# Performance work log

Measured on AMD Instinct MI355X. Metric: run time of the kernel, lower is better.

## Reference

```python
import jax, jax.numpy as jnp
import numpy as np

EPS = 0.05
ITERS = 100
TOL = 1e-4
LN_EPS = 1e-5


def _ln(x, s, b):
    m = x.mean(-1, keepdims=True)
    v = ((x - m) ** 2).mean(-1, keepdims=True)
    return (x - m) / jnp.sqrt(v + LN_EPS) * s + b


def _sinkhorn(M):
    # M: [N, HW] raw logits (fp32). Entropic OT with uniform marginals.
    n, hw = M.shape
    log_K = M / EPS
    log_mu = jnp.log(1.0 / n + 1e-8)
    log_nu = jnp.log(1.0 / hw + 1e-8)

    def cond(st):
        i, lu, lv, diff = st
        return (i < ITERS) & (diff >= TOL)

    def body(st):
        i, lu, lv, _ = st
        new_lu = log_mu - jax.scipy.special.logsumexp(log_K + lv[None, :], axis=1)
        new_lv = log_nu - jax.scipy.special.logsumexp(log_K + new_lu[:, None], axis=0)
        return (i + 1, new_lu, new_lv, jnp.max(jnp.abs(new_lu - lu)))

    st0 = (jnp.int32(0), jnp.zeros((n,), jnp.float32), jnp.zeros((hw,), jnp.float32), jnp.float32(jnp.inf))
    _, lu, lv, _ = jax.lax.while_loop(cond, body, st0)
    log_T = lu[:, None] + log_K + lv[None, :]
    return jnp.clip(jnp.exp(log_T), 0.0, 1.0)


def setup_inputs() -> dict:
    key = jax.random.key(0)
    ks = jax.random.split(key, 12)
    B, C, H, W, N = 16, 256, 64, 64, 5
    E = 2 * C
    w = lambda k, sh: (jax.random.normal(k, sh, jnp.float32) * 0.02)
    return {
        'Fd': jax.random.normal(ks[0], (B, C, H, W), jnp.float32),
        'prompts': w(ks[1], (N, C)),
        'sa_q_w': w(ks[2], (C, C)), 'sa_q_b': jnp.zeros((C,), jnp.float32),
        'sa_k_w': w(ks[3], (C, C)), 'sa_k_b': jnp.zeros((C,), jnp.float32),
        'sa_v_w': w(ks[4], (C, C)), 'sa_v_b': jnp.zeros((C,), jnp.float32),
        'sa_ln_s': jnp.ones((C,), jnp.float32), 'sa_ln_b': jnp.zeros((C,), jnp.float32),
        'wq_w': w(ks[5], (C, C)), 'wq_b': jnp.zeros((C,), jnp.float32),
        'wk_w': w(ks[6], (C, C)), 'wk_b': jnp.zeros((C,), jnp.float32),
        'wv_w': w(ks[7], (C, C)), 'wv_b': jnp.zeros((C,), jnp.float32),
        'ca_ln_s': jnp.ones((C,), jnp.float32), 'ca_ln_b': jnp.zeros((C,), jnp.float32),
        'ffn_w1': w(ks[8], (C, E)), 'ffn_b1': jnp.zeros((E,), jnp.float32),
        'ffn_w2': w(ks[9], (E, C)), 'ffn_b2': jnp.zeros((C,), jnp.float32),
        'ffn_ln_s': jnp.ones((C,), jnp.float32), 'ffn_ln_b': jnp.zeros((C,), jnp.float32),
    }


def reference(Fd, prompts, sa_q_w, sa_q_b, sa_k_w, sa_k_b, sa_v_w, sa_v_b,
              sa_ln_s, sa_ln_b, wq_w, wq_b, wk_w, wk_b, wv_w, wv_b,
              ca_ln_s, ca_ln_b, ffn_w1, ffn_b1, ffn_w2, ffn_b2, ffn_ln_s, ffn_ln_b):
    B, C, H, W = Fd.shape
    scale = C ** -0.5
    Fd_flat = Fd.transpose(0, 2, 3, 1).reshape(B, H * W, C)  # [B, HW, C]
    P = jnp.broadcast_to(prompts[None], (B,) + prompts.shape)  # [B, N, C]

    # self-attention over prompts
    Q = P @ sa_q_w + sa_q_b
    K = P @ sa_k_w + sa_k_b
    V = P @ sa_v_w + sa_v_b
    attn = jax.nn.softmax(jnp.einsum('bnc,bmc->bnm', Q, K) * scale, axis=-1)
    P = _ln(P + jnp.einsum('bnm,bmc->bnc', attn, V), sa_ln_s, sa_ln_b)

    # cross-attention prompts -> pixels
    Qc = P @ wq_w + wq_b                 # [B, N, C]
    Kc = Fd_flat @ wk_w + wk_b           # [B, HW, C]
    Vc = Fd_flat @ wv_w + wv_b           # [B, HW, C]
    logits = jnp.einsum('bnc,bmc->bnm', Qc, Kc) * scale  # [B, N, HW]
    M = jax.nn.softmax(logits, axis=-1)
    P = _ln(P + jnp.einsum('bnm,bmc->bnc', M, Vc), ca_ln_s, ca_ln_b)

    # OT regularization: Sinkhorn on detached logits, BCE(M, T*)
    T = jax.vmap(_sinkhorn)(jax.lax.stop_gradient(logits))
    Mc = jnp.clip(M, 1e-6, 1.0 - 1e-6)
    bce = -(T * jnp.log(Mc) + (1.0 - T) * jnp.log(1.0 - Mc))
    L_ot = bce.mean(axis=(1, 2)).mean()

    # FFN + residual + LN
    h = jax.nn.gelu(P @ ffn_w1 + ffn_b1, approximate=False) @ ffn_w2 + ffn_b2
    P_hat = _ln(P + h, ffn_ln_s, ffn_ln_b)
    return (P_hat, L_ot)
```

## Files before the change

kernel.cpp:

```cpp
#include <hip/hip_runtime.h>
#include <hip/hip_fp16.h>
#include <math.h>

#define LOG2E 1.44269504088896340f
#define LN2   0.69314718055994531f

__device__ __forceinline__ float warpReduceSum(float v){
#pragma unroll
    for (int off = 32; off > 0; off >>= 1) v += __shfl_down(v, off);
    return v;
}
__device__ __forceinline__ float warpReduceMax(float v){
#pragma unroll
    for (int off = 32; off > 0; off >>= 1) v = fmaxf(v, __shfl_down(v, off));
    return v;
}

__device__ float blockSum256(float v, float* s4){
    v = warpReduceSum(v);
    int w = threadIdx.x >> 6;
    __syncthreads();
    if ((threadIdx.x & 63) == 0) s4[w] = v;
    __syncthreads();
    return s4[0] + s4[1] + s4[2] + s4[3];
}
__device__ float blockSum512(float v, float* s8){
    v = warpReduceSum(v);
    int w = threadIdx.x >> 6;
    __syncthreads();
    if ((threadIdx.x & 63) == 0) s8[w] = v;
    __syncthreads();
    float s = 0.f;
#pragma unroll
    for (int i = 0; i < 8; i++) s += s8[i];
    return s;
}

__global__ __launch_bounds__(256) void k_qkv(
    const float* __restrict__ prompts,
    const float* __restrict__ qw, const float* __restrict__ qb,
    const float* __restrict__ kw, const float* __restrict__ kb,
    const float* __restrict__ vw, const float* __restrict__ vb,
    float* __restrict__ QKV)
{
    __shared__ float Pl[1280];
    __shared__ float parts[4][5][64];
    int t = threadIdx.x;
    int mat = blockIdx.x >> 2, chunk = blockIdx.x & 3;
    for (int i = t; i < 1280; i += 256) Pl[i] = prompts[i];
    const float* W  = (mat == 0) ? qw : (mat == 1) ? kw : vw;
    const float* Bv = (mat == 0) ? qb : (mat == 1) ? kb : vb;
    int cl = t & 63, p = t >> 6;
    int col = chunk*64 + cl;
    __syncthreads();
    float acc[5] = {0,0,0,0,0};
    const float* wp = W + (size_t)(p*64)*256 + col;
#pragma unroll 8
    for (int c = 0; c < 64; c++){
        float wv = wp[(size_t)c*256];
#pragma unroll
        for (int n = 0; n < 5; n++) acc[n] += Pl[n*256 + p*64 + c] * wv;
    }
#pragma unroll
    for (int n = 0; n < 5; n++) parts[p][n][cl] = acc[n];
    __syncthreads();
    for (int i = t; i < 320; i += 256){
        int n = i >> 6, c2 = i & 63;
        float s = parts[0][n][c2] + parts[1][n][c2] + parts[2][n][c2] + parts[3][n][c2]
                + Bv[chunk*64 + c2];
        QKV[mat*1280 + n*256 + chunk*64 + c2] = s;
    }
}

__global__ __launch_bounds__(256) void k_attn_qc(
    const float* __restrict__ QKV, const float* __restrict__ prompts,
    const float* __restrict__ lns, const float* __restrict__ lnb,
    const float* __restrict__ wqw, const float* __restrict__ wqb,
    float* __restrict__ P1g, float* __restrict__ Qcg)
{
    __shared__ float Pl[1280], Ql[1280], Kl[1280], Vl[1280], Sl[25], s4[4];
    int t = threadIdx.x;
    for (int i = t; i < 1280; i += 256){
        Pl[i] = prompts[i];
        Ql[i] = QKV[i];
        Kl[i] = QKV[1280 + i];
        Vl[i] = QKV[2560 + i];
    }
    __syncthreads();
    if (t < 25){
        int n = t / 5, m = t % 5;
        float s = 0.f;
        for (int c = 0; c < 256; c++) s += Ql[n*256 + c] * Kl[m*256 + c];
        Sl[t] = s * 0.0625f;
    }
    __syncthreads();
    if (t < 5){
        float mx = -1e30f;
        for (int m = 0; m < 5; m++) mx = fmaxf(mx, Sl[t*5 + m]);
        float e[5], sm = 0.f;
        for (int m = 0; m < 5; m++){ e[m] = expf(Sl[t*5 + m] - mx); sm += e[m]; }
        for (int m = 0; m < 5; m++) Sl[t*5 + m] = e[m] / sm;
    }
    __syncthreads();
    float x[5];
#pragma unroll
    for (int n = 0; n < 5; n++){
        float s = 0.f;
        for (int m = 0; m < 5; m++) s += Sl[n*5 + m] * Vl[m*256 + t];
        x[n] = Pl[n*256 + t] + s;
    }
#pragma unroll
    for (int n = 0; n < 5; n++){
        float sum  = blockSum256(x[n], s4);
        float mean = sum * (1.0f/256.0f);
        float d    = x[n] - mean;
        float sq   = blockSum256(d*d, s4);
        float rstd = rsqrtf(sq * (1.0f/256.0f) + 1e-5f);
        float y = d * rstd * lns[t] + lnb[t];
        Pl[n*256 + t] = y;
        if (blockIdx.x == 0) P1g[n*256 + t] = y;
    }
    __syncthreads();
    int n = blockIdx.x;
    float acc = wqb[t];
    const float* wp = wqw + t;
#pragma unroll 16
    for (int d = 0; d < 256; d++) acc += Pl[n*256 + d] * wp[(size_t)d*256];
    Qcg[n*256 + t] = acc;
}

__global__ __launch_bounds__(256) void k_qk2(
    const float* __restrict__ Qc, const float* __restrict__ wkw,
    const float* __restrict__ wkb,
    float* __restrict__ qkg, float* __restrict__ qkbg)
{
    __shared__ float Qr[256], s4[4];
    int n = blockIdx.y, t = threadIdx.x;
    int w = t >> 6, lane = t & 63;
    Qr[t] = Qc[n*256 + t];
    __syncthreads();
#pragma unroll
    for (int i = 0; i < 4; i++){
        int c = blockIdx.x*16 + w*4 + i;
        const float* kp = wkw + (size_t)c*256;
        float acc = Qr[lane]       * kp[lane]
                  + Qr[lane + 64]  * kp[lane + 64]
                  + Qr[lane + 128] * kp[lane + 128]
                  + Qr[lane + 192] * kp[lane + 192];
#pragma unroll
        for (int off = 1; off < 64; off <<= 1) acc += __shfl_xor(acc, off);
        if (lane == 0) qkg[n*256 + c] = acc;
    }
    if (blockIdx.x == 0){
        float pu = blockSum256(Qr[t] * wkb[t], s4);
        if (t == 0) qkbg[n] = pu;
    }
}

__global__ __launch_bounds__(1024) void k_logits(
    const float* __restrict__ Fd, const float* __restrict__ qkg,
    const float* __restrict__ qkbg, float* __restrict__ logits)
{
    __shared__ float qk[1280];
    __shared__ float qb5[5];
    __shared__ float parts[4][5][256];
    int t = threadIdx.x;
    for (int i = t; i < 1280; i += 1024) qk[i] = qkg[i];
    if (t < 5) qb5[t] = qkbg[t];
    __syncthreads();
    int b = blockIdx.y;
    int p = t >> 8, ml = t & 255;
    int m = blockIdx.x * 256 + ml;
    const float* fp = Fd + ((size_t)(b*256 + p*64)) * 4096 + m;
    float a0 = 0.f, a1 = 0.f, a2 = 0.f, a3 = 0.f, a4 = 0.f;
#pragma unroll 16
    for (int c = 0; c < 64; c++){
        float f = fp[(size_t)c * 4096];
        a0 += qk[          p*64 + c] * f;
        a1 += qk[256  +    p*64 + c] * f;
        a2 += qk[512  +    p*64 + c] * f;
        a3 += qk[768  +    p*64 + c] * f;
        a4 += qk[1024 +    p*64 + c] * f;
    }
    parts[p][0][ml] = a0; parts[p][1][ml] = a1; parts[p][2][ml] = a2;
    parts[p][3][ml] = a3; parts[p][4][ml] = a4;
    __syncthreads();
    for (int i = t; i < 1280; i += 1024){
        int n = i >> 8, mm = i & 255;
        float s = parts[0][n][mm] + parts[1][n][mm] + parts[2][n][mm] + parts[3][n][mm]
                + qb5[n];
        logits[((size_t)(b*5) + n)*4096 + blockIdx.x*256 + mm] = s * 0.0625f;
    }
}

__global__ __launch_bounds__(1024) void k_A(
    const float* __restrict__ Fd, const float* __restrict__ logits,
    float* __restrict__ A)
{
    __shared__ __align__(16) __half Ml[5*4096];
    __shared__ float red[80];
    int b = blockIdx.y, cc = blockIdx.x, t = threadIdx.x;
    int w = t >> 6, lane = t & 63;
    const float* Lb = logits + (size_t)(b*5) * 4096;
    float ll[5][4];
#pragma unroll
    for (int n = 0; n < 5; n++)
#pragma unroll
        for (int k = 0; k < 4; k++)
            ll[n][k] = Lb[n*4096 + t + k*1024];
#pragma unroll
    for (int n = 0; n < 5; n++){
        float tm = fmaxf(fmaxf(ll[n][0], ll[n][1]), fmaxf(ll[n][2], ll[n][3]));
        tm = warpReduceMax(tm);
        if (lane == 0) red[w*5 + n] = tm;
    }
    __syncthreads();
    float mx[5];
#pragma unroll
    for (int n = 0; n < 5; n++){
        float gm = -1e30f;
        for (int i = 0; i < 16; i++) gm = fmaxf(gm, red[i*5 + n]);
        mx[n] = gm;
    }
    __syncthreads();
    float e[5][4];
#pragma unroll
    for (int n = 0; n < 5; n++){
        float ps = 0.f;
#pragma unroll
        for (int k = 0; k < 4; k++){ e[n][k] = expf(ll[n][k] - mx[n]); ps += e[n][k]; }
        ps = warpReduceSum(ps);
        if (lane == 0) red[w*5 + n] = ps;
    }
    __syncthreads();
#pragma unroll
    for (int n = 0; n < 5; n++){
        float z = 0.f;
        for (int i = 0; i < 16; i++) z += red[i*5 + n];
        float inv = 1.0f / z;
#pragma unroll
        for (int k = 0; k < 4; k++)
            Ml[n*4096 + t + k*1024] = __float2half(e[n][k] * inv);
    }
    __syncthreads();
    int c = cc*16 + w;
    const float* fp = Fd + ((size_t)(b*256 + c)) * 4096;
    float4 a4[5];
#pragma unroll
    for (int n = 0; n < 5; n++) a4[n] = make_float4(0.f, 0.f, 0.f, 0.f);
#pragma unroll 4
    for (int it = 0; it < 16; it++){
        int m4 = it*256 + (lane << 2);
        float4 f = *(const float4*)(fp + m4);
#pragma unroll
        for (int n = 0; n < 5; n++){
            const __half2* mp = (const __half2*)(Ml + n*4096 + m4);
            float2 m0 = __half22float2(mp[0]);
            float2 m1 = __half22float2(mp[1]);
            a4[n].x += m0.x * f.x; a4[n].y += m0.y * f.y;
            a4[n].z += m1.x * f.z; a4[n].w += m1.y * f.w;
        }
    }
#pragma unroll
    for (int n = 0; n < 5; n++){
        float s = a4[n].x + a4[n].y + a4[n].z + a4[n].w;
        s = warpReduceSum(s);
        if (lane == 0) A[(size_t)(b*5 + n)*256 + c] = s;
    }
}

__global__ __launch_bounds__(1024) void k_sinkhorn(
    const float* __restrict__ logits, float* __restrict__ partial)
{
    __shared__ __align__(16) float redm[2][5][16];
    __shared__ __align__(16) float reds[5][16];
    __shared__ float redb[16];
    int b = blockIdx.x, t = threadIdx.x;
    int w = t >> 6, lane = t & 63;
    const float* Lb = logits + (size_t)b * 5 * 4096;
    float lk2[5][4], ek[5][4];
#pragma unroll
    for (int n = 0; n < 5; n++)
#pragma unroll
        for (int k = 0; k < 4; k++){
            float lv = (Lb[n*4096 + t + k*1024] / 0.05f) * LOG2E;
            lk2[n][k] = lv;
            ek[n][k] = exp2f(lv);
        }
    const float mu_lin  = 0.2f + 1e-8f;
    const float nu_lin  = 1.0f/4096.0f + 1e-8f;
    const float thr     = 1.00005e-4f;

    float vv[4]  = {1.f, 1.f, 1.f, 1.f};
    float en_prev[5] = {1.f, 1.f, 1.f, 1.f, 1.f};
    float en[5];
    float diff = 1e30f;
    int par = 0;

    for (int it = 0; it < 100; ++it){
        if (diff < 0.f) break;
        float gs[5];
#pragma unroll
        for (int n = 0; n < 5; n++)
            gs[n] = ek[n][0]*vv[0] + ek[n][1]*vv[1] + ek[n][2]*vv[2] + ek[n][3]*vv[3];
#pragma unroll
        for (int off = 1; off < 64; off <<= 1){
#pragma unroll
            for (int n = 0; n < 5; n++) gs[n] += __shfl_xor(gs[n], off);
        }
        if (lane == 0){
#pragma unroll
            for (int n = 0; n < 5; n++) redm[par][n][w] = gs[n];
        }
        __syncthreads();
        float slack = -1.f;
#pragma unroll
        for (int n = 0; n < 5; n++){
            const float4* rp = (const float4*)redm[par][n];
            float4 A4 = rp[0], B4 = rp[1], C4 = rp[2], D4 = rp[3];
            float s = (((A4.x+A4.y)+(A4.z+A4.w)) + ((B4.x+B4.y)+(B4.z+B4.w)))
                    + (((C4.x+C4.y)+(C4.z+C4.w)) + ((D4.x+D4.y)+(D4.z+D4.w)));
            float e = mu_lin / s;
            slack = fmaxf(slack, fabsf(e - en_prev[n]) - thr * en_prev[n]);
            en_prev[n] = e;
            en[n] = e;
        }
        diff = slack;
#pragma unroll
        for (int k = 0; k < 4; k++){
            float cs = ek[0][k]*en[0] + ek[1][k]*en[1] + ek[2][k]*en[2]
                     + ek[3][k]*en[3] + ek[4][k]*en[4];
            vv[k] = nu_lin / cs;
        }
        par ^= 1;
    }
    __syncthreads();

    float tm[5];
#pragma unroll
    for (int n = 0; n < 5; n++){
        float l0 = lk2[n][0]*0.05f, l1 = lk2[n][1]*0.05f;
        float l2 = lk2[n][2]*0.05f, l3 = lk2[n][3]*0.05f;
        tm[n] = fmaxf(fmaxf(l0, l1), fmaxf(l2, l3));
    }
#pragma unroll
    for (int off = 1; off < 64; off <<= 1){
#pragma unroll
        for (int n = 0; n < 5; n++) tm[n] = fmaxf(tm[n], __shfl_xor(tm[n], off));
    }
    if (lane == 0){
#pragma unroll
        for (int n = 0; n < 5; n++) redm[0][n][w] = tm[n];
    }
    __syncthreads();
    float mx5[5];
#pragma unroll
    for (int n = 0; n < 5; n++){
        const float4* rp = (const float4*)redm[0][n];
        float4 A4 = rp[0], B4 = rp[1], C4 = rp[2], D4 = rp[3];
        float gm = fmaxf(fmaxf(fmaxf(A4.x,A4.y), fmaxf(A4.z,A4.w)),
                         fmaxf(fmaxf(B4.x,B4.y), fmaxf(B4.z,B4.w)));
        gm = fmaxf(gm, fmaxf(fmaxf(fmaxf(C4.x,C4.y), fmaxf(C4.z,C4.w)),
                             fmaxf(fmaxf(D4.x,D4.y), fmaxf(D4.z,D4.w))));
        mx5[n] = gm;
    }
    float pz[5];
#pragma unroll
    for (int n = 0; n < 5; n++){
        pz[n] = exp2f(lk2[n][0]*0.05f - mx5[n]) + exp2f(lk2[n][1]*0.05f - mx5[n])
              + exp2f(lk2[n][2]*0.05f - mx5[n]) + exp2f(lk2[n][3]*0.05f - mx5[n]);
    }
#pragma unroll
    for (int off = 1; off < 64; off <<= 1){
#pragma unroll
        for (int n = 0; n < 5; n++) pz[n] += __shfl_xor(pz[n], off);
    }
    if (lane == 0){
#pragma unroll
        for (int n = 0; n < 5; n++) reds[n][w] = pz[n];
    }
    __syncthreads();
    float iz5[5];
#pragma unroll
    for (int n = 0; n < 5; n++){
        const float4* rp = (const float4*)reds[n];
        float4 A4 = rp[0], B4 = rp[1], C4 = rp[2], D4 = rp[3];
        float z = (((A4.x+A4.y)+(A4.z+A4.w)) + ((B4.x+B4.y)+(B4.z+B4.w)))
                + (((C4.x+C4.y)+(C4.z+C4.w)) + ((D4.x+D4.y)+(D4.z+D4.w)));
        iz5[n] = 1.0f / z;
    }
    float acc = 0.f;
#pragma unroll
    for (int n = 0; n < 5; n++){
#pragma unroll
        for (int k = 0; k < 4; k++){
            float Mv = exp2f(lk2[n][k]*0.05f - mx5[n]) * iz5[n];
            float Mc = fminf(fmaxf(Mv, 1e-6f), 1.0f - 1e-6f);
            float T  = fminf(en[n] * ek[n][k] * vv[k], 1.0f);
            acc -= (T * log2f(Mc) + (1.0f - T) * log2f(1.0f - Mc)) * LN2;
        }
    }
    acc = warpReduceSum(acc);
    if (lane == 0) redb[w] = acc;
    __syncthreads();
    if (t == 0){
        float s = 0.f;
        for (int i = 0; i < 16; i++) s += redb[i];
        partial[b] = s;
    }
}

__global__ __launch_bounds__(512) void k_epilogue(
    const float* __restrict__ A, const float* __restrict__ P1,
    const float* __restrict__ wvw, const float* __restrict__ wvb,
    const float* __restrict__ clns, const float* __restrict__ clnb,
    const float* __restrict__ w1, const float* __restrict__ b1,
    const float* __restrict__ w2, const float* __restrict__ b2,
    const float* __restrict__ flns, const float* __restrict__ flnb,
    const float* __restrict__ sink_part,
    float* __restrict__ out)
{
    __shared__ float Ar[256], P1r[256], P2[256], hl[512], parts[2][256], s8[8];
    int bn = blockIdx.x;
    int n = bn % 5;
    int t = threadIdx.x;
    if (bn == 0 && t == 0){
        float s = 0.f;
        for (int i = 0; i < 16; i++) s += sink_part[i];
        out[20480] = s * (1.0f / (16.0f * 5.0f * 4096.0f));
    }
    if (t < 256){ Ar[t] = A[(size_t)bn*256 + t]; P1r[t] = P1[n*256 + t]; }
    __syncthreads();
    int c = t & 255, p = t >> 8;
    {
        float acc = 0.f;
        const float* wp = wvw + (size_t)(p*128)*256 + c;
#pragma unroll 16
        for (int k = 0; k < 128; k++) acc += Ar[p*128 + k] * wp[(size_t)k*256];
        parts[p][c] = acc;
    }
    __syncthreads();
    float x = 0.f;
    if (t < 256) x = P1r[t] + parts[0][t] + parts[1][t] + wvb[t];
    float sum  = blockSum512((t < 256) ? x : 0.f, s8);
    float mean = sum * (1.0f/256.0f);
    float d    = x - mean;
    float sq   = blockSum512((t < 256) ? d*d : 0.f, s8);
    float rstd = rsqrtf(sq * (1.0f/256.0f) + 1e-5f);
    float p2v = 0.f;
    if (t < 256){
        p2v = d * rstd * clns[t] + clnb[t];
        P2[t] = p2v;
    }
    __syncthreads();
    {
        float a = b1[t];
        const float* wp = w1 + t;
#pragma unroll 16
        for (int k = 0; k < 256; k++) a += P2[k] * wp[(size_t)k*512];
        hl[t] = 0.5f * a * (1.0f + erff(a * 0.70710678118654752f));
    }
    __syncthreads();
    {
        float acc = 0.f;
        const float* wp = w2 + (size_t)(p*256)*256 + c;
#pragma unroll 16
        for (int k = 0; k < 256; k++) acc += hl[p*256 + k] * wp[(size_t)k*256];
        parts[p][c] = acc;
    }
    __syncthreads();
    float x2 = 0.f;
    if (t < 256) x2 = P2[t] + parts[0][t] + parts[1][t] + b2[t];
    float sum2  = blockSum512((t < 256) ? x2 : 0.f, s8);
    float mean2 = sum2 * (1.0f/256.0f);
    float d2    = x2 - mean2;
    float sq2   = blockSum512((t < 256) ? d2*d2 : 0.f, s8);
    float rstd2 = rsqrtf(sq2 * (1.0f/256.0f) + 1e-5f);
    if (t < 256) out[(size_t)bn*256 + t] = d2 * rstd2 * flns[t] + flnb[t];
}

extern "C" void kernel_launch(void* const* d_in, const int* in_sizes, int n_in,
                              void* d_out, int out_size, void* d_ws, size_t ws_size,
                              hipStream_t stream)
{
    const float* Fd      = (const float*)d_in[0];
    const float* prompts = (const float*)d_in[1];
    const float* sa_q_w  = (const float*)d_in[2];
    const float* sa_q_b  = (const float*)d_in[3];
    const float* sa_k_w  = (const float*)d_in[4];
    const float* sa_k_b  = (const float*)d_in[5];
    const float* sa_v_w  = (const float*)d_in[6];
    const float* sa_v_b  = (const float*)d_in[7];
    const float* sa_ln_s = (const float*)d_in[8];
    const float* sa_ln_b = (const float*)d_in[9];
    const float* wq_w    = (const float*)d_in[10];
    const float* wq_b    = (const float*)d_in[11];
    const float* wk_w    = (const float*)d_in[12];
    const float* wk_b    = (const float*)d_in[13];
    const float* wv_w    = (const float*)d_in[14];
    const float* wv_b    = (const float*)d_in[15];
    const float* ca_ln_s = (const float*)d_in[16];
    const float* ca_ln_b = (const float*)d_in[17];
    const float* ffn_w1  = (const float*)d_in[18];
    const float* ffn_b1  = (const float*)d_in[19];
    const float* ffn_w2  = (const float*)d_in[20];
    const float* ffn_b2  = (const float*)d_in[21];
    const float* ffn_ln_s= (const float*)d_in[22];
    const float* ffn_ln_b= (const float*)d_in[23];

    float* out = (float*)d_out;
    float* ws  = (float*)d_ws;

    float* P1     = ws;
    float* qkb    = ws + 1536;
    float* QKV    = ws + 2048;
    float* Qc     = ws + 6144;
    float* qkg    = ws + 8192;
    float* spart  = ws + 9472;
    float* logits = ws + 73728;
    float* Amat   = ws + 401408;

    k_qkv<<<12, 256, 0, stream>>>(prompts, sa_q_w, sa_q_b, sa_k_w, sa_k_b,
                                  sa_v_w, sa_v_b, QKV);
    k_attn_qc<<<5, 256, 0, stream>>>(QKV, prompts, sa_ln_s, sa_ln_b,
                                     wq_w, wq_b, P1, Qc);
    k_qk2<<<dim3(16, 5), 256, 0, stream>>>(Qc, wk_w, wk_b, qkg, qkb);
    k_logits<<<dim3(16, 16), 1024, 0, stream>>>(Fd, qkg, qkb, logits);
    k_A<<<dim3(16, 16), 1024, 0, stream>>>(Fd, logits, Amat);
    k_sinkhorn<<<16, 1024, 0, stream>>>(logits, spart);
    k_epilogue<<<80, 512, 0, stream>>>(Amat, P1, wv_w, wv_b, ca_ln_s, ca_ln_b,
                                       ffn_w1, ffn_b1, ffn_w2, ffn_b2,
                                       ffn_ln_s, ffn_ln_b, spart, out);
}
```

Measured before the change: 247.1 us.

## Merge Sinkhorn into k_A launch so both run concurrently, use fast reciprocal

Combines the Sinkhorn kernel and the A-matrix kernel into one 272-block launch. The first 16 blocks run Sinkhorn and the rest compute A, so the latency-bound serial Sinkhorn loop overlaps with the bandwidth-bound A pass. It also replaces the per-iteration float4 LDS reductions with 16-lane shuffle reductions, and uses hardware rcp in place of IEEE division. The fast reciprocal slightly changes numerics. The merged kernel's shared memory footprint now applies to both block types.

Result: faster. 218.7 us (-11.5%).

```diff
diff --git a/kernel.cpp b/kernel.cpp
--- a/kernel.cpp
+++ b/kernel.cpp
@@ -4,6 +4,8 @@
 
 #define LOG2E 1.44269504088896340f
 #define LN2   0.69314718055994531f
+
+__device__ __forceinline__ float fastrcp(float x){ return __builtin_amdgcn_rcpf(x); }
 
 __device__ __forceinline__ float warpReduceSum(float v){
 #pragma unroll
@@ -193,14 +195,165 @@
     }
 }
 
-__global__ __launch_bounds__(1024) void k_A(
+__global__ __launch_bounds__(1024) void k_A_sink(
     const float* __restrict__ Fd, const float* __restrict__ logits,
-    float* __restrict__ A)
+    float* __restrict__ A, float* __restrict__ partial)
 {
     __shared__ __align__(16) __half Ml[5*4096];
     __shared__ float red[80];
-    int b = blockIdx.y, cc = blockIdx.x, t = threadIdx.x;
+    __shared__ __align__(16) float redm[2][5][16];
+    __shared__ float redb[16];
+    int t = threadIdx.x;
     int w = t >> 6, lane = t & 63;
+
+    if (blockIdx.x < 16){
+        int b = blockIdx.x;
+        const float* Lb = logits + (size_t)b * 5 * 4096;
+        float lk2[5][4], ek[5][4];
+#pragma unroll
+        for (int n = 0; n < 5; n++)
+#pragma unroll
+            for (int k = 0; k < 4; k++){
+                float lv = (Lb[n*4096 + t + k*1024] * 20.0f) * LOG2E;
+                lk2[n][k] = lv;
+                ek[n][k] = exp2f(lv);
+            }
+        const float mu_lin  = 0.2f + 1e-8f;
+        const float nu_lin  = 1.0f/4096.0f + 1e-8f;
+        const float thr     = 1.00005e-4f;
+
+        float vv[4]  = {1.f, 1.f, 1.f, 1.f};
+        float en_prev[5] = {1.f, 1.f, 1.f, 1.f, 1.f};
+        float en[5];
+        float diff = 1e30f;
+        int par = 0;
+
+        for (int it = 0; it < 100; ++it){
+            if (diff < 0.f) break;
+            float gs[5];
+#pragma unroll
+            for (int n = 0; n < 5; n++)
+                gs[n] = ek[n][0]*vv[0] + ek[n][1]*vv[1] + ek[n][2]*vv[2] + ek[n][3]*vv[3];
+#pragma unroll
+            for (int off = 1; off < 64; off <<= 1){
+#pragma unroll
+                for (int n = 0; n < 5; n++) gs[n] += __shfl_xor(gs[n], off);
+            }
+            if (lane == 0){
+#pragma unroll
+                for (int n = 0; n < 5; n++) redm[par][n][w] = gs[n];
+            }
+            __syncthreads();
+            float s5[5];
+            int g = lane & 15;
+#pragma unroll
+            for (int n = 0; n < 5; n++) s5[n] = redm[par][n][g];
+#pragma unroll
+            for (int off = 1; off < 16; off <<= 1){
+#pragma unroll
+                for (int n = 0; n < 5; n++) s5[n] += __shfl_xor(s5[n], off);
+            }
+            float slack = -1.f;
+#pragma unroll
+            for (int n = 0; n < 5; n++){
+                float e = mu_lin * fastrcp(s5[n]);
+                slack = fmaxf(slack, fabsf(e - en_prev[n]) - thr * en_prev[n]);
+                en_prev[n] = e;
+                en[n] = e;
+            }
+            diff = slack;
+#pragma unroll
+            for (int k = 0; k < 4; k++){
+                float cs = ek[0][k]*en[0] + ek[1][k]*en[1] + ek[2][k]*en[2]
+                         + ek[3][k]*en[3] + ek[4][k]*en[4];
+                vv[k] = nu_lin * fastrcp(cs);
+            }
+            par ^= 1;
+        }
+        __syncthreads();
+
+        float tm[5];
+#pragma unroll
+        for (int n = 0; n < 5; n++){
+            float l0 = lk2[n][0]*0.05f, l1 = lk2[n][1]*0.05f;
+            float l2 = lk2[n][2]*0.05f, l3 = lk2[n][3]*0.05f;
+            tm[n] = fmaxf(fmaxf(l0, l1), fmaxf(l2, l3));
+        }
+#pragma unroll
+        for (int off = 1; off < 64; off <<= 1){
+#pragma unroll
+            for (int n = 0; n < 5; n++) tm[n] = fmaxf(tm[n], __shfl_xor(tm[n], off));
+        }
+        if (lane == 0){
+#pragma unroll
+            for (int n = 0; n < 5; n++) redm[0][n][w] = tm[n];
+        }
+        __syncthreads();
+        float mx5[5];
+        {
+            int g = lane & 15;
+#pragma unroll
+            for (int n = 0; n < 5; n++) mx5[n] = redm[0][n][g];
+#pragma unroll
+            for (int off = 1; off < 16; off <<= 1){
+#pragma unroll
+                for (int n = 0; n < 5; n++) mx5[n] = fmaxf(mx5[n], __shfl_xor(mx5[n], off));
+            }
+        }
+        float pz[5];
+#pragma unroll
+        for (int n = 0; n < 5; n++){
+            pz[n] = exp2f(lk2[n][0]*0.05f - mx5[n]) + exp2f(lk2[n][1]*0.05f - mx5[n])
+                  + exp2f(lk2[n][2]*0.05f - mx5[n]) + exp2f(lk2[n][3]*0.05f - mx5[n]);
+        }
+#pragma unroll
+        for (int off = 1; off < 64; off <<= 1){
+#pragma unroll
+            for (int n = 0; n < 5; n++) pz[n] += __shfl_xor(pz[n], off);
+        }
+        __syncthreads();
+        if (lane == 0){
+#pragma unroll
+            for (int n = 0; n < 5; n++) redm[1][n][w] = pz[n];
+        }
+        __syncthreads();
+        float iz5[5];
+        {
+            int g = lane & 15;
+#pragma unroll
+            for (int n = 0; n < 5; n++) iz5[n] = redm[1][n][g];
+#pragma unroll
+            for (int off = 1; off < 16; off <<= 1){
+#pragma unroll
+                for (int n = 0; n < 5; n++) iz5[n] += __shfl_xor(iz5[n], off);
+            }
+#pragma unroll
+            for (int n = 0; n < 5; n++) iz5[n] = fastrcp(iz5[n]);
+        }
+        float acc = 0.f;
+#pragma unroll
+        for (int n = 0; n < 5; n++){
+#pragma unroll
+            for (int k = 0; k < 4; k++){
+                float Mv = exp2f(lk2[n][k]*0.05f - mx5[n]) * iz5[n];
+                float Mc = fminf(fmaxf(Mv, 1e-6f), 1.0f - 1e-6f);
+                float T  = fminf(en[n] * ek[n][k] * vv[k], 1.0f);
+                acc -= (T * log2f(Mc) + (1.0f - T) * log2f(1.0f - Mc)) * LN2;
+            }
+        }
+        acc = warpReduceSum(acc);
+        if (lane == 0) redb[w] = acc;
+        __syncthreads();
+        if (t == 0){
+            float s = 0.f;
+            for (int i = 0; i < 16; i++) s += redb[i];
+            partial[b] = s;
+        }
+        return;
+    }
+
+    int bid = blockIdx.x - 16;
+    int b = bid >> 4, cc = bid & 15;
     const float* Lb = logits + (size_t)(b*5) * 4096;
     float ll[5][4];
 #pragma unroll
@@ -266,147 +419,6 @@
         float s = a4[n].x + a4[n].y + a4[n].z + a4[n].w;
         s = warpReduceSum(s);
         if (lane == 0) A[(size_t)(b*5 + n)*256 + c] = s;
-    }
-}
-
-__global__ __launch_bounds__(1024) void k_sinkhorn(
-    const float* __restrict__ logits, float* __restrict__ partial)
-{
-    __shared__ __align__(16) float redm[2][5][16];
-    __shared__ __align__(16) float reds[5][16];
-    __shared__ float redb[16];
-    int b = blockIdx.x, t = threadIdx.x;
-    int w = t >> 6, lane = t & 63;
-    const float* Lb = logits + (size_t)b * 5 * 4096;
-    float lk2[5][4], ek[5][4];
-#pragma unroll
-    for (int n = 0; n < 5; n++)
-#pragma unroll
-        for (int k = 0; k < 4; k++){
-            float lv = (Lb[n*4096 + t + k*1024] / 0.05f) * LOG2E;
-            lk2[n][k] = lv;
-            ek[n][k] = exp2f(lv);
-        }
-    const float mu_lin  = 0.2f + 1e-8f;
-    const float nu_lin  = 1.0f/4096.0f + 1e-8f;
-    const float thr     = 1.00005e-4f;
-
-    float vv[4]  = {1.f, 1.f, 1.f, 1.f};
-    float en_prev[5] = {1.f, 1.f, 1.f, 1.f, 1.f};
-    float en[5];
-    float diff = 1e30f;
-    int par = 0;
-
-    for (int it = 0; it < 100; ++it){
-        if (diff < 0.f) break;
-        float gs[5];
-#pragma unroll
-        for (int n = 0; n < 5; n++)
-            gs[n] = ek[n][0]*vv[0] + ek[n][1]*vv[1] + ek[n][2]*vv[2] + ek[n][3]*vv[3];
-#pragma unroll
-        for (int off = 1; off < 64; off <<= 1){
-#pragma unroll
-            for (int n = 0; n < 5; n++) gs[n] += __shfl_xor(gs[n], off);
-        }
-        if (lane == 0){
-#pragma unroll
-            for (int n = 0; n < 5; n++) redm[par][n][w] = gs[n];
-        }
-        __syncthreads();
-        float slack = -1.f;
-#pragma unroll
-        for (int n = 0; n < 5; n++){
-            const float4* rp = (const float4*)redm[par][n];
-            float4 A4 = rp[0], B4 = rp[1], C4 = rp[2], D4 = rp[3];
-            float s = (((A4.x+A4.y)+(A4.z+A4.w)) + ((B4.x+B4.y)+(B4.z+B4.w)))
-                    + (((C4.x+C4.y)+(C4.z+C4.w)) + ((D4.x+D4.y)+(D4.z+D4.w)));
-            float e = mu_lin / s;
-            slack = fmaxf(slack, fabsf(e - en_prev[n]) - thr * en_prev[n]);
-            en_prev[n] = e;
-            en[n] = e;
-        }
-        diff = slack;
-#pragma unroll
-        for (int k = 0; k < 4; k++){
-            float cs = ek[0][k]*en[0] + ek[1][k]*en[1] + ek[2][k]*en[2]
-                     + ek[3][k]*en[3] + ek[4][k]*en[4];
-            vv[k] = nu_lin / cs;
-        }
-        par ^= 1;
-    }
-    __syncthreads();
-
-    float tm[5];
-#pragma unroll
-    for (int n = 0; n < 5; n++){
-        float l0 = lk2[n][0]*0.05f, l1 = lk2[n][1]*0.05f;
-        float l2 = lk2[n][2]*0.05f, l3 = lk2[n][3]*0.05f;
-        tm[n] = fmaxf(fmaxf(l0, l1), fmaxf(l2, l3));
-    }
-#pragma unroll
-    for (int off = 1; off < 64; off <<= 1){
-#pragma unroll
-        for (int n = 0; n < 5; n++) tm[n] = fmaxf(tm[n], __shfl_xor(tm[n], off));
-    }
-    if (lane == 0){
-#pragma unroll
-        for (int n = 0; n < 5; n++) redm[0][n][w] = tm[n];
-    }
-    __syncthreads();
-    float mx5[5];
-#pragma unroll
-    for (int n = 0; n < 5; n++){
-        const float4* rp = (const float4*)redm[0][n];
-        float4 A4 = rp[0], B4 = rp[1], C4 = rp[2], D4 = rp[3];
-        float gm = fmaxf(fmaxf(fmaxf(A4.x,A4.y), fmaxf(A4.z,A4.w)),
-                         fmaxf(fmaxf(B4.x,B4.y), fmaxf(B4.z,B4.w)));
-        gm = fmaxf(gm, fmaxf(fmaxf(fmaxf(C4.x,C4.y), fmaxf(C4.z,C4.w)),
-                             fmaxf(fmaxf(D4.x,D4.y), fmaxf(D4.z,D4.w))));
-        mx5[n] = gm;
-    }
-    float pz[5];
-#pragma unroll
-    for (int n = 0; n < 5; n++){
-        pz[n] = exp2f(lk2[n][0]*0.05f - mx5[n]) + exp2f(lk2[n][1]*0.05f - mx5[n])
-              + exp2f(lk2[n][2]*0.05f - mx5[n]) + exp2f(lk2[n][3]*0.05f - mx5[n]);
-    }
-#pragma unroll
-    for (int off = 1; off < 64; off <<= 1){
-#pragma unroll
-        for (int n = 0; n < 5; n++) pz[n] += __shfl_xor(pz[n], off);
-    }
-    if (lane == 0){
-#pragma unroll
-        for (int n = 0; n < 5; n++) reds[n][w] = pz[n];
-    }
-    __syncthreads();
-    float iz5[5];
-#pragma unroll
-    for (int n = 0; n < 5; n++){
-        const float4* rp = (const float4*)reds[n];
-        float4 A4 = rp[0], B4 = rp[1], C4 = rp[2], D4 = rp[3];
-        float z = (((A4.x+A4.y)+(A4.z+A4.w)) + ((B4.x+B4.y)+(B4.z+B4.w)))
-                + (((C4.x+C4.y)+(C4.z+C4.w)) + ((D4.x+D4.y)+(D4.z+D4.w)));
-        iz5[n] = 1.0f / z;
-    }
-    float acc = 0.f;
-#pragma unroll
-    for (int n = 0; n < 5; n++){
-#pragma unroll
-        for (int k = 0; k < 4; k++){
-            float Mv = exp2f(lk2[n][k]*0.05f - mx5[n]) * iz5[n];
-            float Mc = fminf(fmaxf(Mv, 1e-6f), 1.0f - 1e-6f);
-            float T  = fminf(en[n] * ek[n][k] * vv[k], 1.0f);
-            acc -= (T * log2f(Mc) + (1.0f - T) * log2f(1.0f - Mc)) * LN2;
-        }
-    }
-    acc = warpReduceSum(acc);
-    if (lane == 0) redb[w] = acc;
-    __syncthreads();
-    if (t == 0){
-        float s = 0.f;
-        for (int i = 0; i < 16; i++) s += redb[i];
-        partial[b] = s;
     }
 }
 
@@ -526,8 +538,7 @@
                                      wq_w, wq_b, P1, Qc);
     k_qk2<<<dim3(16, 5), 256, 0, stream>>>(Qc, wk_w, wk_b, qkg, qkb);
     k_logits<<<dim3(16, 16), 1024, 0, stream>>>(Fd, qkg, qkb, logits);
-    k_A<<<dim3(16, 16), 1024, 0, stream>>>(Fd, logits, Amat);
-    k_sinkhorn<<<16, 1024, 0, stream>>>(logits, spart);
+    k_A_sink<<<272, 1024, 0, stream>>>(Fd, logits, Amat, spart);
     k_epilogue<<<80, 512, 0, stream>>>(Amat, P1, wv_w, wv_b, ca_ln_s, ca_ln_b,
                                        ffn_w1, ffn_b1, ffn_w2, ffn_b2,
                                        ffn_ln_s, ffn_ln_b, spart, out);
```
